# Performance work log

Measured on AMD Instinct MI355X. Metric: run time of the kernel, lower is better.

Reference implementation:

```python
import jax, jax.numpy as jnp
import numpy as np

B, S, D = 4, 2048, 1024
H, HD = 16, 64  # num_heads, head_size
NEG = -1e20


def setup_inputs() -> dict:
    key = jax.random.key(0)
    ks = jax.random.split(key, 8)
    query = jax.random.normal(ks[0], (B, S, D), dtype=jnp.float32)
    k_in = jax.random.normal(ks[1], (B, S, D), dtype=jnp.float32)
    v_in = jax.random.normal(ks[2], (B, S, D), dtype=jnp.float32)
    # causal mask: True where attention is DISALLOWED (masked_fill semantics)
    mask = jnp.triu(jnp.ones((S, S), dtype=bool), k=1)
    scale = 1.0 / np.sqrt(D)
    Wq = jax.random.normal(ks[3], (D, H * HD), dtype=jnp.float32) * scale
    Wk = jax.random.normal(ks[4], (D, H * HD), dtype=jnp.float32) * scale
    Wv = jax.random.normal(ks[5], (D, H * HD), dtype=jnp.float32) * scale
    Wo = jax.random.normal(ks[6], (H * HD, D), dtype=jnp.float32) * scale
    bo = jnp.zeros((D,), dtype=jnp.float32)
    return {"query": query, "key": k_in, "value": v_in, "mask": mask,
            "Wq": Wq, "Wk": Wk, "Wv": Wv, "Wo": Wo, "bo": bo}


def reference(query, key, value, mask, Wq, Wk, Wv, Wo, bo):
    # projections -> [B, H, S, HD]
    q = (query @ Wq).reshape(B, -1, H, HD).transpose(0, 2, 1, 3)
    k = (key @ Wk).reshape(B, -1, H, HD).transpose(0, 2, 1, 3)
    v = (value @ Wv).reshape(B, -1, H, HD).transpose(0, 2, 1, 3)
    # scaled dot-product attention with boolean mask (True = masked out)
    scores = jnp.einsum('bhqd,bhkd->bhqk', q, k) / jnp.sqrt(jnp.float32(HD))
    scores = jnp.where(mask, jnp.float32(NEG), scores)
    attn = jax.nn.softmax(scores, axis=-1)
    out = jnp.einsum('bhqk,bhkd->bhqd', attn, v)  # [B,H,S,HD]
    out = out.transpose(0, 2, 1, 3).reshape(B, -1, H * HD)
    return out @ Wo + bo
```

## Files before the change

### kernel.cpp

```cpp
#include <hip/hip_runtime.h>

#define B_ 4
#define S_ 2048
#define D_ 1024
#define H_ 16
#define HD_ 64

typedef __attribute__((ext_vector_type(8))) short bf16x8;
typedef __attribute__((ext_vector_type(4))) float f32x4;
typedef __attribute__((ext_vector_type(4))) unsigned u32x4;

__device__ __forceinline__ short f2bf(float f) {
  unsigned u = __builtin_bit_cast(unsigned, f);
  u += 0x7fffu + ((u >> 16) & 1u);
  return (short)(u >> 16);
}

__device__ __forceinline__ unsigned cvtpk(float a, float b) {
  unsigned r;
  asm("v_cvt_pk_bf16_f32 %0, %1, %2" : "=v"(r) : "v"(a), "v"(b));
  return r;
}

__device__ __forceinline__ void gload_lds16(const void* g, void* l) {
  __builtin_amdgcn_global_load_lds((const __attribute__((address_space(1))) void*)g,
                                   (__attribute__((address_space(3))) void*)l, 16, 0, 0);
}

__device__ __forceinline__ bf16x8 ldsw8(const short* base, int row, int colb) {
  const int off = (row * 128 + colb) ^ ((row & 7) << 4);
  return *(const bf16x8*)((const char*)base + off);
}

__device__ __forceinline__ int bpr_off(int row, int cbyte) {
  return ((row >> 1) << 7) + ((((row & 1) << 6) + cbyte) ^ (((row >> 1) & 7) << 4));
}

#define MFMA16(a, b, c) __builtin_amdgcn_mfma_f32_16x16x32_bf16((a), (b), (c), 0, 0, 0)
#define PBAR()   asm volatile("s_barrier" ::: "memory")
#define LGKM0()  do { asm volatile("s_waitcnt lgkmcnt(0)" ::: "memory"); \
                      __builtin_amdgcn_sched_barrier(0); } while (0)
#define VM0()    asm volatile("s_waitcnt vmcnt(0)" ::: "memory")

__global__ void transpose_cast_w4(const float* __restrict__ W0, const float* __restrict__ W1,
                                  const float* __restrict__ W2, const float* __restrict__ W3,
                                  short* __restrict__ T0, short* __restrict__ T1,
                                  short* __restrict__ T2, short* __restrict__ T3) {
  __shared__ float tile[32][33];
  const int z = blockIdx.z;
  const float* W = z == 0 ? W0 : z == 1 ? W1 : z == 2 ? W2 : W3;
  short* Wt = z == 0 ? T0 : z == 1 ? T1 : z == 2 ? T2 : T3;
  const int n0 = blockIdx.x * 32, k0 = blockIdx.y * 32;
  const int tx = threadIdx.x, ty = threadIdx.y;
  #pragma unroll
  for (int i = ty; i < 32; i += 8)
    tile[i][tx] = W[(size_t)(k0 + i) * 1024 + n0 + tx];
  __syncthreads();
  #pragma unroll
  for (int i = ty; i < 32; i += 8)
    Wt[(size_t)(n0 + i) * 1024 + k0 + tx] = f2bf(tile[tx][i]);
}

__global__ __launch_bounds__(512, 2) void gemm8(const float* __restrict__ Aq,
                                                const float* __restrict__ Ak,
                                                const float* __restrict__ Av,
                                                const short* __restrict__ Bq,
                                                const short* __restrict__ Bk,
                                                const short* __restrict__ Bv,
                                                short* __restrict__ Oq,
                                                short* __restrict__ Ok,
                                                short* __restrict__ Ov,
                                                float qscale) {
  __shared__ __align__(16) float AsF[2][16384];
  __shared__ __align__(16) short BsS[16384];
  const int z = blockIdx.z;
  const float* A = z == 0 ? Aq : z == 1 ? Ak : Av;
  const short* Bt = z == 0 ? Bq : z == 1 ? Bk : Bv;
  short* outb = z == 0 ? Oq : z == 1 ? Ok : Ov;
  const float oscale = (z == 0) ? qscale : 1.0f;

  const int tid = threadIdx.x;
  const int l = tid & 63, w = tid >> 6;
  const int wm = w >> 2, wn = w & 3;
  const int l15 = l & 15, lq = l >> 4;
  const int flat = blockIdx.x + (blockIdx.y << 2);
  const int vid = (flat & 7) * 16 + (flat >> 3);
  const int row0 = (vid >> 2) * 256;
  const int col0 = (vid & 3) * 256;

  f32x4 acc[8][4] = {};

  auto stageB = [&](int kt) {
    #pragma unroll
    for (int j = 0; j < 4; ++j) {
      const int o2 = w * 4096 + j * 1024 + l * 16;
      const int row = o2 >> 7;
      const int sc = (o2 & 127) ^ ((row & 7) << 4);
      gload_lds16((const char*)Bt + (size_t)(col0 + row) * 2048 + kt * 128 + sc,
                  (char*)BsS + o2);
    }
  };
  auto stageA = [&](int kt, int buf, int batch) {
    #pragma unroll
    for (int j = 0; j < 4; ++j) {
      const int o2 = w * 8192 + (batch * 4 + j) * 1024 + l * 16;
      const int row = o2 >> 8;
      const int sc = (o2 & 255) ^ ((row & 7) << 4);
      gload_lds16((const char*)A + (size_t)(row0 + row) * 4096 + kt * 256 + sc,
                  (char*)AsF[buf] + o2);
    }
  };
  auto rdA = [&](const float* as, int R, int ks) -> bf16x8 {
    const int s = (R & 7) << 4;
    const int c0 = (ks * 128 + lq * 32) ^ s;
    const f32x4 g0 = *(const f32x4*)((const char*)as + R * 256 + c0);
    const f32x4 g1 = *(const f32x4*)((const char*)as + R * 256 + (c0 ^ 16));
    const u32x4 uu = {cvtpk(g0[0], g0[1]), cvtpk(g0[2], g0[3]),
                      cvtpk(g1[0], g1[1]), cvtpk(g1[2], g1[3])};
    return __builtin_bit_cast(bf16x8, uu);
  };

  stageB(0);
  stageA(0, 0, 0);
  stageA(0, 0, 1);
  VM0();
  PBAR();

  for (int t = 0; t < 16; ++t) {
    const int c = t & 1, o = c ^ 1;
    const float* Ah = AsF[c];
    bf16x8 bfr[4][2];

    #pragma unroll
    for (int p = 0; p < 4; ++p) {
      if (p == 1 && t + 1 < 16) { stageB(t + 1); stageA(t + 1, o, 0); }
      if (p == 2 && t + 1 < 16) stageA(t + 1, o, 1);

      if (p == 0) {
        #pragma unroll
        for (int nf = 0; nf < 4; ++nf)
          #pragma unroll
          for (int ks = 0; ks < 2; ++ks)
            bfr[nf][ks] = ldsw8(BsS, wn * 64 + nf * 16 + l15, ks * 64 + lq * 16);
      }
      const bf16x8 a00 = rdA(Ah, wm * 128 + (2 * p) * 16 + l15, 0);
      const bf16x8 a01 = rdA(Ah, wm * 128 + (2 * p) * 16 + l15, 1);
      const bf16x8 a10 = rdA(Ah, wm * 128 + (2 * p + 1) * 16 + l15, 0);
      const bf16x8 a11 = rdA(Ah, wm * 128 + (2 * p + 1) * 16 + l15, 1);

      LGKM0();
      __builtin_amdgcn_s_setprio(1);
      #pragma unroll
      for (int nf = 0; nf < 4; ++nf) {
        acc[2 * p][nf]     = MFMA16(a00, bfr[nf][0], acc[2 * p][nf]);
        acc[2 * p][nf]     = MFMA16(a01, bfr[nf][1], acc[2 * p][nf]);
        acc[2 * p + 1][nf] = MFMA16(a10, bfr[nf][0], acc[2 * p + 1][nf]);
        acc[2 * p + 1][nf] = MFMA16(a11, bfr[nf][1], acc[2 * p + 1][nf]);
      }
      __builtin_amdgcn_s_setprio(0);
      if (p < 3) PBAR();
    }
    if (t + 1 < 16) { VM0(); PBAR(); }
  }

  #pragma unroll
  for (int mf = 0; mf < 8; ++mf) {
    #pragma unroll
    for (int nf = 0; nf < 4; ++nf) {
      #pragma unroll
      for (int r = 0; r < 4; ++r) {
        const int gr = row0 + wm * 128 + mf * 16 + lq * 4 + r;
        const int gc = col0 + wn * 64 + nf * 16 + l15;
        const float v = acc[mf][nf][r];
        const int b = gr >> 11, s = gr & 2047;
        const int h = gc >> 6, hd = gc & 63;
        if (z < 2)
          outb[(((size_t)(b * H_ + h)) * S_ + s) * HD_ + hd] = f2bf(v * oscale);
        else
          outb[(((size_t)(b * H_ + h)) * HD_ + hd) * S_ + s] = f2bf(v);
      }
    }
  }
}

__global__ __launch_bounds__(256) void gemm_o(const short* __restrict__ A,
                                              const short* __restrict__ Bt,
                                              float* __restrict__ outf,
                                              const float* __restrict__ bias) {
  __shared__ __align__(16) short As[2][128 * 32];
  __shared__ __align__(16) short Bs[2][128 * 32];
  const int tid = threadIdx.x;
  const int l = tid & 63;
  const int w = tid >> 6;
  const int wm = w >> 1, wn = w & 1;
  const int flat = blockIdx.x + (blockIdx.y << 3);
  const int xcd = flat & 7, t = flat >> 3;
  const int row0 = (xcd * 8 + (t & 7)) * 128;
  const int col0 = (t >> 3) * 128;
  const int l15 = l & 15, lq = l >> 4;

  f32x4 acc[4][4] = {};

  auto stage = [&](const short* src, int r0, int k0, short* lds) {
    #pragma unroll
    for (int i = 0; i < 2; i++) {
      const int o = w * 2048 + i * 1024 + l * 16;
      const int row2 = o >> 7;
      const int ip = (o & 127) ^ ((row2 & 7) << 4);
      const int row = row2 * 2 + (ip >> 6);
      const int cb = ip & 63;
      gload_lds16((const char*)src + ((size_t)(r0 + row) * 1024 + k0) * 2 + cb,
                  (char*)lds + o);
    }
  };

  stage(A, row0, 0, As[0]);
  stage(Bt, col0, 0, Bs[0]);

  for (int kt = 0; kt < 32; ++kt) {
    __syncthreads();
    if (kt + 1 < 32) {
      stage(A, row0, (kt + 1) * 32, As[(kt + 1) & 1]);
      stage(Bt, col0, (kt + 1) * 32, Bs[(kt + 1) & 1]);
    }
    const short* as = As[kt & 1];
    const short* bs = Bs[kt & 1];
    bf16x8 af[4], bfv[4];
    #pragma unroll
    for (int mf = 0; mf < 4; mf++)
      af[mf] = *(const bf16x8*)((const char*)as + bpr_off(wm * 64 + mf * 16 + l15, lq * 16));
    #pragma unroll
    for (int nf = 0; nf < 4; nf++)
      bfv[nf] = *(const bf16x8*)((const char*)bs + bpr_off(wn * 64 + nf * 16 + l15, lq * 16));
    #pragma unroll
    for (int mf = 0; mf < 4; mf++)
      #pragma unroll
      for (int nf = 0; nf < 4; nf++)
        acc[mf][nf] = MFMA16(af[mf], bfv[nf], acc[mf][nf]);
  }

  #pragma unroll
  for (int mf = 0; mf < 4; mf++)
    #pragma unroll
    for (int nf = 0; nf < 4; nf++)
      #pragma unroll
      for (int r = 0; r < 4; r++) {
        const int gr = row0 + wm * 64 + mf * 16 + lq * 4 + r;
        const int gc = col0 + wn * 64 + nf * 16 + l15;
        outf[(size_t)gr * 1024 + gc] = acc[mf][nf][r] + bias[gc];
      }
}

__global__ __launch_bounds__(256) void attn_kernel(const short* __restrict__ Qh,
                                                   const short* __restrict__ Kh,
                                                   const short* __restrict__ Vtr,
                                                   short* __restrict__ attnout) {
  __shared__ __align__(16) short Ks[2][64 * 64];
  __shared__ __align__(16) short Vs[2][64 * 64];
  __shared__ __align__(16) short Ps[4][32 * 64];
  const int tid = threadIdx.x, l = tid & 63, w = tid >> 6;
  const int l15 = l & 15, lq = l >> 4;
  const int flat = blockIdx.x;
  const int vid = (flat & 7) * 64 + (flat >> 3);
  const int bh = vid >> 3, pairx = vid & 7;
  const int b = bh >> 4, h = bh & 15;
  const size_t base = (size_t)bh * (S_ * HD_);
  const short* Qp = Qh + base;
  const short* Kp = Kh + base;
  const short* Vp = Vtr + base;
  short* Pw = (short*)Ps[w];

  for (int pass = 0; pass < 2; ++pass) {
    const int qt = pass ? 15 - pairx : pairx;
    const int q0 = qt * 128;
    const int qw = q0 + w * 32;
    const int nkt = (q0 >> 6) + 2;

    bf16x8 qf[2][2];
    #pragma unroll
    for (int qh = 0; qh < 2; qh++)
      #pragma unroll
      for (int ks = 0; ks < 2; ks++)
        qf[qh][ks] = *(const bf16x8*)(Qp + (size_t)(qw + qh * 16 + l15) * 64 + ks * 32 + lq * 8);

    f32x4 oacc[4][2] = {};
    float mrow[2] = {-1e30f, -1e30f};
    float lpart[2] = {0.f, 0.f};

    auto stage = [&](int kt, int bf) {
      const int k0s = kt << 6;
      #pragma unroll
      for (int i = 0; i < 2; i++) {
        const int o = w * 2048 + i * 1024 + l * 16;
        const int sw = o ^ (((o >> 7) & 7) << 4);
        gload_lds16((const char*)Kp + (size_t)k0s * 128 + sw, (char*)Ks[bf] + o);
        gload_lds16(Vp + (size_t)(o >> 7) * S_ + k0s + ((sw & 127) >> 1), (char*)Vs[bf] + o);
      }
    };

    stage(0, 0);
    __syncthreads();

    for (int kt = 0; kt < nkt; ++kt) {
      const int cur = kt & 1;
      if (kt + 1 < nkt) stage(kt + 1, cur ^ 1);
      const int k0 = kt << 6;

      if (k0 <= qw + 31) {
        f32x4 sacc[2][4] = {};
        __builtin_amdgcn_s_setprio(1);
        #pragma unroll
        for (int ks = 0; ks < 2; ks++) {
          #pragma unroll
          for (int mf = 0; mf < 4; mf++) {
            const bf16x8 kf = ldsw8(Ks[cur], mf * 16 + l15, ks * 64 + lq * 16);
            #pragma unroll
            for (int qh = 0; qh < 2; qh++)
              sacc[qh][mf] = MFMA16(kf, qf[qh][ks], sacc[qh][mf]);
          }
        }
        __builtin_amdgcn_s_setprio(0);

        if (k0 + 63 > qw) {
          #pragma unroll
          for (int qh = 0; qh < 2; qh++) {
            const int qg = qw + qh * 16 + l15 - lq * 4;
            #pragma unroll
            for (int mf = 0; mf < 4; mf++)
              #pragma unroll
              for (int r = 0; r < 4; r++)
                if (k0 + mf * 16 + r > qg) sacc[qh][mf][r] = -1e30f;
          }
        }

        float mxl[2];
        #pragma unroll
        for (int qh = 0; qh < 2; qh++) {
          float m = fmaxf(fmaxf(sacc[qh][0][0], sacc[qh][0][1]),
                          fmaxf(sacc[qh][0][2], sacc[qh][0][3]));
          #pragma unroll
          for (int mf = 1; mf < 4; mf++)
            m = fmaxf(m, fmaxf(fmaxf(sacc[qh][mf][0], sacc[qh][mf][1]),
                               fmaxf(sacc[qh][mf][2], sacc[qh][mf][3])));
          mxl[qh] = m;
        }

        const bool need = (mxl[0] > mrow[0] + 8.f) || (mxl[1] > mrow[1] + 8.f);
        if (__any(need)) {
          #pragma unroll
          for (int qh = 0; qh < 2; qh++) {
            float m = fmaxf(mxl[qh], __shfl_xor(mxl[qh], 16));
            m = fmaxf(m, __shfl_xor(m, 32));
            const float mn = fmaxf(mrow[qh], m);
            const float fac = __builtin_amdgcn_exp2f(mrow[qh] - mn);
            mrow[qh] = mn;
            lpart[qh] *= fac;
            #pragma unroll
            for (int mf = 0; mf < 4; mf++) oacc[mf][qh] *= fac;
          }
        }

        #pragma unroll
        for (int qh = 0; qh < 2; qh++) {
          float rs = 0.f;
          const int row = qh * 16 + l15;
          #pragma unroll
          for (int mf = 0; mf < 4; mf++) {
            f32x4 p;
            #pragma unroll
            for (int r = 0; r < 4; r++) {
              const float e = __builtin_amdgcn_exp2f(sacc[qh][mf][r] - mrow[qh]);
              p[r] = e;
              rs += e;
            }
            const int off = (row * 128 + mf * 32 + lq * 8) ^ ((row & 7) << 4);
            *(uint2*)((char*)Pw + off) = make_uint2(cvtpk(p[0], p[1]), cvtpk(p[2], p[3]));
          }
          lpart[qh] += rs;
        }

        asm volatile("s_waitcnt lgkmcnt(0)" ::: "memory");
        __builtin_amdgcn_sched_barrier(0);

        __builtin_amdgcn_s_setprio(1);
        #pragma unroll
        for (int ks = 0; ks < 2; ks++) {
          bf16x8 pb[2];
          #pragma unroll
          for (int qh = 0; qh < 2; qh++) {
            const int row = qh * 16 + l15;
            const int off = (row * 128 + ks * 64 + lq * 16) ^ ((row & 7) << 4);
            pb[qh] = *(const bf16x8*)((const char*)Pw + off);
          }
          #pragma unroll
          for (int mf = 0; mf < 4; mf++) {
            const bf16x8 vf = ldsw8(Vs[cur], mf * 16 + l15, ks * 64 + lq * 16);
            #pragma unroll
            for (int qh = 0; qh < 2; qh++)
              oacc[mf][qh] = MFMA16(vf, pb[qh], oacc[mf][qh]);
          }
        }
        __builtin_amdgcn_s_setprio(0);
      }
      __syncthreads();
    }

    #pragma unroll
    for (int qh = 0; qh < 2; qh++) {
      float lr = lpart[qh];
      lr += __shfl_xor(lr, 16);
      lr += __shfl_xor(lr, 32);
      const float rinv = __builtin_amdgcn_rcpf(lr);
      const int q = qw + qh * 16 + l15;
      #pragma unroll
      for (int mf = 0; mf < 4; mf++) {
        const f32x4 o = oacc[mf][qh];
        const uint2 u = make_uint2(cvtpk(o[0] * rinv, o[1] * rinv),
                                   cvtpk(o[2] * rinv, o[3] * rinv));
        *(uint2*)(attnout + ((size_t)b * S_ + q) * (H_ * HD_) + h * 64 + mf * 16 + lq * 4) = u;
      }
    }
  }
}

extern "C" void kernel_launch(void* const* d_in, const int* in_sizes, int n_in,
                              void* d_out, int out_size, void* d_ws, size_t ws_size,
                              hipStream_t stream) {
  const float* query = (const float*)d_in[0];
  const float* key_  = (const float*)d_in[1];
  const float* value = (const float*)d_in[2];
  const float* Wq = (const float*)d_in[4];
  const float* Wk = (const float*)d_in[5];
  const float* Wv = (const float*)d_in[6];
  const float* Wo = (const float*)d_in[7];
  const float* bo = (const float*)d_in[8];
  float* out = (float*)d_out;

  char* ws = (char*)d_ws;
  const size_t MB = (size_t)1 << 20;
  short* Xbuf = (short*)(ws);
  short* Wqt  = (short*)(ws + 16 * MB);
  short* Wkt  = (short*)(ws + 18 * MB);
  short* Wvt  = (short*)(ws + 20 * MB);
  short* Wot  = (short*)(ws + 22 * MB);
  short* Qh   = (short*)(ws + 24 * MB);
  short* Kh   = (short*)(ws + 40 * MB);
  short* Vt   = (short*)(ws + 56 * MB);

  const dim3 tb(32, 8);
  const dim3 tg4(32, 32, 4);
  const float QSCALE = 0.125f * 1.4426950408889634f;

  transpose_cast_w4<<<tg4, tb, 0, stream>>>(Wq, Wk, Wv, Wo, Wqt, Wkt, Wvt, Wot);

  gemm8<<<dim3(4, 32, 3), 512, 0, stream>>>(query, key_, value, Wqt, Wkt, Wvt,
                                            Qh, Kh, Vt, QSCALE);

  attn_kernel<<<dim3(512), 256, 0, stream>>>(Qh, Kh, Vt, Xbuf);

  gemm_o<<<dim3(8, 64), 256, 0, stream>>>(Xbuf, Wot, out, bo);
}
```

Baseline: 243.4 us.

## Restructure QKV projection GEMM to 256x128 tiles with double-buffered B and vmcnt pipelining

The QKV projection GEMM tile goes from 256x256 to 256x128, which doubles the grid to 768 blocks, and the wave layout becomes 4x2 with 4x4 accumulators per wave. B tiles are now double-buffered and prefetched two steps ahead. Full vmcnt(0) drains are replaced with partial vmcnt(2) waits, so global-to-LDS loads stay in flight across iterations and there are fewer barriers per k-step. The aim is better load balance across CUs and more overlap of memory with MFMA, at the cost of lower per-block data reuse and one block per CU given the LDS footprint.

```diff
diff --git a/kernel.cpp b/kernel.cpp
--- a/kernel.cpp
+++ b/kernel.cpp
@@ -40,7 +40,6 @@
 #define PBAR()   asm volatile("s_barrier" ::: "memory")
 #define LGKM0()  do { asm volatile("s_waitcnt lgkmcnt(0)" ::: "memory"); \
                       __builtin_amdgcn_sched_barrier(0); } while (0)
-#define VM0()    asm volatile("s_waitcnt vmcnt(0)" ::: "memory")
 
 __global__ void transpose_cast_w4(const float* __restrict__ W0, const float* __restrict__ W1,
                                   const float* __restrict__ W2, const float* __restrict__ W3,
@@ -61,18 +60,18 @@
     Wt[(size_t)(n0 + i) * 1024 + k0 + tx] = f2bf(tile[tx][i]);
 }
 
-__global__ __launch_bounds__(512, 2) void gemm8(const float* __restrict__ Aq,
-                                                const float* __restrict__ Ak,
-                                                const float* __restrict__ Av,
-                                                const short* __restrict__ Bq,
-                                                const short* __restrict__ Bk,
-                                                const short* __restrict__ Bv,
-                                                short* __restrict__ Oq,
-                                                short* __restrict__ Ok,
-                                                short* __restrict__ Ov,
-                                                float qscale) {
+__global__ __launch_bounds__(512, 1) void gemm_qkv8(const float* __restrict__ Aq,
+                                                    const float* __restrict__ Ak,
+                                                    const float* __restrict__ Av,
+                                                    const short* __restrict__ Bq,
+                                                    const short* __restrict__ Bk,
+                                                    const short* __restrict__ Bv,
+                                                    short* __restrict__ Oq,
+                                                    short* __restrict__ Ok,
+                                                    short* __restrict__ Ov,
+                                                    float qscale) {
   __shared__ __align__(16) float AsF[2][16384];
-  __shared__ __align__(16) short BsS[16384];
+  __shared__ __align__(16) short Bs[2][8192];
   const int z = blockIdx.z;
   const float* A = z == 0 ? Aq : z == 1 ? Ak : Av;
   const short* Bt = z == 0 ? Bq : z == 1 ? Bk : Bv;
@@ -81,25 +80,15 @@
 
   const int tid = threadIdx.x;
   const int l = tid & 63, w = tid >> 6;
-  const int wm = w >> 2, wn = w & 3;
+  const int wm = w >> 1, wn = w & 1;
   const int l15 = l & 15, lq = l >> 4;
-  const int flat = blockIdx.x + (blockIdx.y << 2);
-  const int vid = (flat & 7) * 16 + (flat >> 3);
-  const int row0 = (vid >> 2) * 256;
-  const int col0 = (vid & 3) * 256;
-
-  f32x4 acc[8][4] = {};
-
-  auto stageB = [&](int kt) {
-    #pragma unroll
-    for (int j = 0; j < 4; ++j) {
-      const int o2 = w * 4096 + j * 1024 + l * 16;
-      const int row = o2 >> 7;
-      const int sc = (o2 & 127) ^ ((row & 7) << 4);
-      gload_lds16((const char*)Bt + (size_t)(col0 + row) * 2048 + kt * 128 + sc,
-                  (char*)BsS + o2);
-    }
-  };
+  const int flat8 = blockIdx.x + (blockIdx.y << 3);
+  const int vid = (flat8 & 7) * 32 + (flat8 >> 3);
+  const int row0 = (vid >> 3) * 256;
+  const int col0 = (vid & 7) * 128;
+
+  f32x4 acc[4][4] = {};
+
   auto stageA = [&](int kt, int buf, int batch) {
     #pragma unroll
     for (int j = 0; j < 4; ++j) {
@@ -110,9 +99,19 @@
                   (char*)AsF[buf] + o2);
     }
   };
+  auto stageB = [&](int kt) {
+    const int buf = kt & 1;
+    #pragma unroll
+    for (int j = 0; j < 2; ++j) {
+      const int o2 = w * 2048 + j * 1024 + l * 16;
+      const int row = o2 >> 7;
+      const int sc = (o2 & 127) ^ ((row & 7) << 4);
+      gload_lds16((const char*)Bt + (size_t)(col0 + row) * 2048 + kt * 128 + sc,
+                  (char*)Bs[buf] + o2);
+    }
+  };
   auto rdA = [&](const float* as, int R, int ks) -> bf16x8 {
-    const int s = (R & 7) << 4;
-    const int c0 = (ks * 128 + lq * 32) ^ s;
+    const int c0 = (ks * 128 + lq * 32) ^ ((R & 7) << 4);
     const f32x4 g0 = *(const f32x4*)((const char*)as + R * 256 + c0);
     const f32x4 g1 = *(const f32x4*)((const char*)as + R * 256 + (c0 ^ 16));
     const u32x4 uu = {cvtpk(g0[0], g0[1]), cvtpk(g0[2], g0[3]),
@@ -120,56 +119,72 @@
     return __builtin_bit_cast(bf16x8, uu);
   };
 
-  stageB(0);
   stageA(0, 0, 0);
   stageA(0, 0, 1);
-  VM0();
-  PBAR();
+  stageB(0);
+  stageB(1);
 
   for (int t = 0; t < 16; ++t) {
     const int c = t & 1, o = c ^ 1;
+    if (t < 15) asm volatile("s_waitcnt vmcnt(2)" ::: "memory");
+    else        asm volatile("s_waitcnt vmcnt(0)" ::: "memory");
+    PBAR();
+
     const float* Ah = AsF[c];
+    const short* Bh = Bs[c];
     bf16x8 bfr[4][2];
 
-    #pragma unroll
-    for (int p = 0; p < 4; ++p) {
-      if (p == 1 && t + 1 < 16) { stageB(t + 1); stageA(t + 1, o, 0); }
-      if (p == 2 && t + 1 < 16) stageA(t + 1, o, 1);
-
-      if (p == 0) {
-        #pragma unroll
-        for (int nf = 0; nf < 4; ++nf)
-          #pragma unroll
-          for (int ks = 0; ks < 2; ++ks)
-            bfr[nf][ks] = ldsw8(BsS, wn * 64 + nf * 16 + l15, ks * 64 + lq * 16);
-      }
-      const bf16x8 a00 = rdA(Ah, wm * 128 + (2 * p) * 16 + l15, 0);
-      const bf16x8 a01 = rdA(Ah, wm * 128 + (2 * p) * 16 + l15, 1);
-      const bf16x8 a10 = rdA(Ah, wm * 128 + (2 * p + 1) * 16 + l15, 0);
-      const bf16x8 a11 = rdA(Ah, wm * 128 + (2 * p + 1) * 16 + l15, 1);
-
+    if (t + 1 < 16) stageA(t + 1, o, 0);
+    #pragma unroll
+    for (int nf = 0; nf < 4; ++nf)
+      #pragma unroll
+      for (int ks = 0; ks < 2; ++ks)
+        bfr[nf][ks] = ldsw8(Bh, wn * 64 + nf * 16 + l15, ks * 64 + lq * 16);
+    {
+      const bf16x8 a00 = rdA(Ah, wm * 64 + 0 * 16 + l15, 0);
+      const bf16x8 a01 = rdA(Ah, wm * 64 + 0 * 16 + l15, 1);
+      const bf16x8 a10 = rdA(Ah, wm * 64 + 1 * 16 + l15, 0);
+      const bf16x8 a11 = rdA(Ah, wm * 64 + 1 * 16 + l15, 1);
       LGKM0();
       __builtin_amdgcn_s_setprio(1);
       #pragma unroll
       for (int nf = 0; nf < 4; ++nf) {
-        acc[2 * p][nf]     = MFMA16(a00, bfr[nf][0], acc[2 * p][nf]);
-        acc[2 * p][nf]     = MFMA16(a01, bfr[nf][1], acc[2 * p][nf]);
-        acc[2 * p + 1][nf] = MFMA16(a10, bfr[nf][0], acc[2 * p + 1][nf]);
-        acc[2 * p + 1][nf] = MFMA16(a11, bfr[nf][1], acc[2 * p + 1][nf]);
+        acc[0][nf] = MFMA16(a00, bfr[nf][0], acc[0][nf]);
+        acc[0][nf] = MFMA16(a01, bfr[nf][1], acc[0][nf]);
+        acc[1][nf] = MFMA16(a10, bfr[nf][0], acc[1][nf]);
+        acc[1][nf] = MFMA16(a11, bfr[nf][1], acc[1][nf]);
       }
       __builtin_amdgcn_s_setprio(0);
-      if (p < 3) PBAR();
-    }
-    if (t + 1 < 16) { VM0(); PBAR(); }
+    }
+    PBAR();
+
+    if (t + 1 < 16) stageA(t + 1, o, 1);
+    if (t + 2 < 16) stageB(t + 2);
+    {
+      const bf16x8 a00 = rdA(Ah, wm * 64 + 2 * 16 + l15, 0);
+      const bf16x8 a01 = rdA(Ah, wm * 64 + 2 * 16 + l15, 1);
+      const bf16x8 a10 = rdA(Ah, wm * 64 + 3 * 16 + l15, 0);
+      const bf16x8 a11 = rdA(Ah, wm * 64 + 3 * 16 + l15, 1);
+      LGKM0();
+      __builtin_amdgcn_s_setprio(1);
+      #pragma unroll
+      for (int nf = 0; nf < 4; ++nf) {
+        acc[2][nf] = MFMA16(a00, bfr[nf][0], acc[2][nf]);
+        acc[2][nf] = MFMA16(a01, bfr[nf][1], acc[2][nf]);
+        acc[3][nf] = MFMA16(a10, bfr[nf][0], acc[3][nf]);
+        acc[3][nf] = MFMA16(a11, bfr[nf][1], acc[3][nf]);
+      }
+      __builtin_amdgcn_s_setprio(0);
+    }
   }
 
   #pragma unroll
-  for (int mf = 0; mf < 8; ++mf) {
+  for (int mf = 0; mf < 4; ++mf) {
     #pragma unroll
     for (int nf = 0; nf < 4; ++nf) {
       #pragma unroll
       for (int r = 0; r < 4; ++r) {
-        const int gr = row0 + wm * 128 + mf * 16 + lq * 4 + r;
+        const int gr = row0 + wm * 64 + mf * 16 + lq * 4 + r;
         const int gc = col0 + wn * 64 + nf * 16 + l15;
         const float v = acc[mf][nf][r];
         const int b = gr >> 11, s = gr & 2047;
@@ -453,8 +468,8 @@
 
   transpose_cast_w4<<<tg4, tb, 0, stream>>>(Wq, Wk, Wv, Wo, Wqt, Wkt, Wvt, Wot);
 
-  gemm8<<<dim3(4, 32, 3), 512, 0, stream>>>(query, key_, value, Wqt, Wkt, Wvt,
-                                            Qh, Kh, Vt, QSCALE);
+  gemm_qkv8<<<dim3(8, 32, 3), 512, 0, stream>>>(query, key_, value, Wqt, Wkt, Wvt,
+                                                Qh, Kh, Vt, QSCALE);
 
   attn_kernel<<<dim3(512), 256, 0, stream>>>(Qh, Kh, Vt, Xbuf);
 
```

Measured after the change: 226.7 us. -6.9%, faster.

## Stage A through registers as bf16 in LDS and deepen B prefetch pipeline

Applied to the files above, without the earlier changes.

The QKV projection GEMM now loads fp32 activations into registers, converts them to bf16 once, and writes the bf16 tile to LDS. It no longer stages fp32 in LDS and converts on every fragment read. LDS use is halved, which allows double-buffered A and two-stage-ahead B prefetch using counted vmcnt waits instead of full drains. A small max-reduction in the attention kernel is also rebalanced into a tree. The change adds register pressure for the prefetched A values and makes the barrier and wait placement more intricate.

```diff
diff --git a/kernel.cpp b/kernel.cpp
--- a/kernel.cpp
+++ b/kernel.cpp
@@ -40,7 +40,6 @@
 #define PBAR()   asm volatile("s_barrier" ::: "memory")
 #define LGKM0()  do { asm volatile("s_waitcnt lgkmcnt(0)" ::: "memory"); \
                       __builtin_amdgcn_sched_barrier(0); } while (0)
-#define VM0()    asm volatile("s_waitcnt vmcnt(0)" ::: "memory")
 
 __global__ void transpose_cast_w4(const float* __restrict__ W0, const float* __restrict__ W1,
                                   const float* __restrict__ W2, const float* __restrict__ W3,
@@ -71,8 +70,7 @@
                                                 short* __restrict__ Ok,
                                                 short* __restrict__ Ov,
                                                 float qscale) {
-  __shared__ __align__(16) float AsF[2][16384];
-  __shared__ __align__(16) short BsS[16384];
+  __shared__ __align__(16) short lds[2][4][8192];
   const int z = blockIdx.z;
   const float* A = z == 0 ? Aq : z == 1 ? Ak : Av;
   const short* Bt = z == 0 ? Bq : z == 1 ? Bk : Bv;
@@ -90,63 +88,74 @@
 
   f32x4 acc[8][4] = {};
 
-  auto stageB = [&](int kt) {
-    #pragma unroll
-    for (int j = 0; j < 4; ++j) {
-      const int o2 = w * 4096 + j * 1024 + l * 16;
+  auto stageB = [&](short* dst, int hrow, int kt) {
+    #pragma unroll
+    for (int j = 0; j < 2; ++j) {
+      const int o2 = w * 1024 + j * 8192 + l * 16;
       const int row = o2 >> 7;
       const int sc = (o2 & 127) ^ ((row & 7) << 4);
-      gload_lds16((const char*)Bt + (size_t)(col0 + row) * 2048 + kt * 128 + sc,
-                  (char*)BsS + o2);
+      gload_lds16((const char*)Bt + ((size_t)(col0 + hrow + row) * 1024 + kt * 64) * 2 + sc,
+                  (char*)dst + o2);
     }
   };
-  auto stageA = [&](int kt, int buf, int batch) {
-    #pragma unroll
-    for (int j = 0; j < 4; ++j) {
-      const int o2 = w * 8192 + (batch * 4 + j) * 1024 + l * 16;
-      const int row = o2 >> 8;
-      const int sc = (o2 & 255) ^ ((row & 7) << 4);
-      gload_lds16((const char*)A + (size_t)(row0 + row) * 4096 + kt * 256 + sc,
-                  (char*)AsF[buf] + o2);
-    }
+  const int arow = tid >> 2;
+  const int acb = (tid & 3) * 32;
+  float4 rA0[4], rA1[4];
+  auto loadAh = [&](float4* r, int hrow, int kt) {
+    const float4* p = (const float4*)(A + (size_t)(row0 + hrow + arow) * 1024 +
+                                      kt * 64 + (tid & 3) * 16);
+    r[0] = p[0]; r[1] = p[1]; r[2] = p[2]; r[3] = p[3];
   };
-  auto rdA = [&](const float* as, int R, int ks) -> bf16x8 {
-    const int s = (R & 7) << 4;
-    const int c0 = (ks * 128 + lq * 32) ^ s;
-    const f32x4 g0 = *(const f32x4*)((const char*)as + R * 256 + c0);
-    const f32x4 g1 = *(const f32x4*)((const char*)as + R * 256 + (c0 ^ 16));
-    const u32x4 uu = {cvtpk(g0[0], g0[1]), cvtpk(g0[2], g0[3]),
-                      cvtpk(g1[0], g1[1]), cvtpk(g1[2], g1[3])};
-    return __builtin_bit_cast(bf16x8, uu);
+  auto writeAh = [&](const float4* r, short* dst) {
+    const u32x4 w0 = {cvtpk(r[0].x, r[0].y), cvtpk(r[0].z, r[0].w),
+                      cvtpk(r[1].x, r[1].y), cvtpk(r[1].z, r[1].w)};
+    const u32x4 w1 = {cvtpk(r[2].x, r[2].y), cvtpk(r[2].z, r[2].w),
+                      cvtpk(r[3].x, r[3].y), cvtpk(r[3].z, r[3].w)};
+    *(u32x4*)((char*)dst + ((arow * 128 + acb) ^ ((arow & 7) << 4))) = w0;
+    *(u32x4*)((char*)dst + ((arow * 128 + acb + 16) ^ ((arow & 7) << 4))) = w1;
   };
 
-  stageB(0);
-  stageA(0, 0, 0);
-  stageA(0, 0, 1);
-  VM0();
-  PBAR();
+  loadAh(rA0, 0, 0);
+  loadAh(rA1, 128, 0);
+  writeAh(rA0, lds[0][0]);
+  writeAh(rA1, lds[0][1]);
+  stageB(lds[0][2], 0, 0);
+  stageB(lds[0][3], 128, 0);
+  stageB(lds[1][2], 0, 1);
+  stageB(lds[1][3], 128, 1);
+  asm volatile("s_waitcnt lgkmcnt(0)" ::: "memory");
 
   for (int t = 0; t < 16; ++t) {
     const int c = t & 1, o = c ^ 1;
-    const float* Ah = AsF[c];
+    if (t < 15) asm volatile("s_waitcnt vmcnt(4)" ::: "memory");
+    else        asm volatile("s_waitcnt vmcnt(0)" ::: "memory");
+    PBAR();
+
+    const short* Ah = lds[c][wm];
+    const short* Bh = lds[c][2 + (wn >> 1)];
+    const int brow = (wn & 1) * 64;
     bf16x8 bfr[4][2];
 
     #pragma unroll
     for (int p = 0; p < 4; ++p) {
-      if (p == 1 && t + 1 < 16) { stageB(t + 1); stageA(t + 1, o, 0); }
-      if (p == 2 && t + 1 < 16) stageA(t + 1, o, 1);
+      if (p == 0 && t + 1 < 16) loadAh(rA0, 0, t + 1);
+      if (p == 1 && t + 1 < 16) loadAh(rA1, 128, t + 1);
+      if (p == 1 && t + 2 < 16) stageB(lds[c][2], 0, t + 2);
+      if (p == 2 && t + 2 < 16) stageB(lds[c][3], 128, t + 2);
+      if (p == 2 && t + 1 < 16) writeAh(rA0, lds[o][0]);
+      if (p == 3 && t + 1 < 16) writeAh(rA1, lds[o][1]);
 
       if (p == 0) {
         #pragma unroll
         for (int nf = 0; nf < 4; ++nf)
           #pragma unroll
           for (int ks = 0; ks < 2; ++ks)
-            bfr[nf][ks] = ldsw8(BsS, wn * 64 + nf * 16 + l15, ks * 64 + lq * 16);
-      }
-      const bf16x8 a00 = rdA(Ah, wm * 128 + (2 * p) * 16 + l15, 0);
-      const bf16x8 a01 = rdA(Ah, wm * 128 + (2 * p) * 16 + l15, 1);
-      const bf16x8 a10 = rdA(Ah, wm * 128 + (2 * p + 1) * 16 + l15, 0);
-      const bf16x8 a11 = rdA(Ah, wm * 128 + (2 * p + 1) * 16 + l15, 1);
+            bfr[nf][ks] = ldsw8(Bh, brow + nf * 16 + l15, ks * 64 + lq * 16);
+      }
+      const bf16x8 a00 = ldsw8(Ah, (2 * p) * 16 + l15, lq * 16);
+      const bf16x8 a01 = ldsw8(Ah, (2 * p) * 16 + l15, 64 + lq * 16);
+      const bf16x8 a10 = ldsw8(Ah, (2 * p + 1) * 16 + l15, lq * 16);
+      const bf16x8 a11 = ldsw8(Ah, (2 * p + 1) * 16 + l15, 64 + lq * 16);
 
       LGKM0();
       __builtin_amdgcn_s_setprio(1);
@@ -158,9 +167,8 @@
         acc[2 * p + 1][nf] = MFMA16(a11, bfr[nf][1], acc[2 * p + 1][nf]);
       }
       __builtin_amdgcn_s_setprio(0);
-      if (p < 3) PBAR();
-    }
-    if (t + 1 < 16) { VM0(); PBAR(); }
+      PBAR();
+    }
   }
 
   #pragma unroll
@@ -336,13 +344,15 @@
         float mxl[2];
         #pragma unroll
         for (int qh = 0; qh < 2; qh++) {
-          float m = fmaxf(fmaxf(sacc[qh][0][0], sacc[qh][0][1]),
-                          fmaxf(sacc[qh][0][2], sacc[qh][0][3]));
-          #pragma unroll
-          for (int mf = 1; mf < 4; mf++)
-            m = fmaxf(m, fmaxf(fmaxf(sacc[qh][mf][0], sacc[qh][mf][1]),
-                               fmaxf(sacc[qh][mf][2], sacc[qh][mf][3])));
-          mxl[qh] = m;
+          float t0 = fmaxf(fmaxf(sacc[qh][0][0], sacc[qh][0][1]),
+                           fmaxf(sacc[qh][0][2], sacc[qh][0][3]));
+          float t1 = fmaxf(fmaxf(sacc[qh][1][0], sacc[qh][1][1]),
+                           fmaxf(sacc[qh][1][2], sacc[qh][1][3]));
+          float t2 = fmaxf(fmaxf(sacc[qh][2][0], sacc[qh][2][1]),
+                           fmaxf(sacc[qh][2][2], sacc[qh][2][3]));
+          float t3 = fmaxf(fmaxf(sacc[qh][3][0], sacc[qh][3][1]),
+                           fmaxf(sacc[qh][3][2], sacc[qh][3][3]));
+          mxl[qh] = fmaxf(fmaxf(t0, t1), fmaxf(t2, t3));
         }
 
         const bool need = (mxl[0] > mrow[0] + 8.f) || (mxl[1] > mrow[1] + 8.f);
```

After: 225.3 us. 1.08x faster.
